# Optimization experiments

Measured on AMD Instinct MI355X. Metric: run time of the kernel, lower is better.

Reference implementation:

```python
import jax, jax.numpy as jnp
import numpy as np

B, S, E, H = 2, 2048, 1024, 16
D = E // H  # head size = 64


def setup_inputs() -> dict:
    key = jax.random.key(0)
    ks = jax.random.split(key, 13)
    scale = 1.0 / np.sqrt(E)
    inp = {
        "q": jax.random.normal(ks[0], (B, S, E), jnp.float32),
        "k": jax.random.normal(ks[1], (B, S, E), jnp.float32),
        "v": jax.random.normal(ks[2], (B, S, E), jnp.float32),
        "mask": jax.random.randint(ks[3], (B, 1, S, S), 0, 2, jnp.int32),
        "Wq": jax.random.normal(ks[4], (E, E), jnp.float32) * scale,
        "bq": jnp.zeros((E,), jnp.float32),
        "Wk": jax.random.normal(ks[5], (E, E), jnp.float32) * scale,
        "bk": jnp.zeros((E,), jnp.float32),
        "Wv": jax.random.normal(ks[6], (E, E), jnp.float32) * scale,
        "bv": jnp.zeros((E,), jnp.float32),
        "Wo": jax.random.normal(ks[7], (E, E), jnp.float32) * scale,
        "bo": jnp.zeros((E,), jnp.float32),
    }
    return inp


def reference(q, k, v, mask, Wq, bq, Wk, bk, Wv, bv, Wo, bo):
    # Linear projections (torch Linear: x @ W.T + b)
    qh = (q @ Wq.T + bq).reshape(B, S, H, D).transpose(0, 2, 1, 3)  # [B,H,S,D]
    kh = (k @ Wk.T + bk).reshape(B, S, H, D).transpose(0, 2, 1, 3)
    vh = (v @ Wv.T + bv).reshape(B, S, H, D).transpose(0, 2, 1, 3)

    scores = jnp.einsum("bhqd,bhkd->bhqk", qh, kh) / jnp.sqrt(jnp.float32(D))
    scores = jnp.where(mask == 0, jnp.float32(-1e10), scores)
    attn = jax.nn.softmax(scores, axis=-1)  # [B,H,S,S]
    ctx = jnp.einsum("bhqk,bhkd->bhqd", attn, vh)  # dropout p=0.0 -> identity

    out = ctx.transpose(0, 2, 1, 3).reshape(B, S, E)
    return out @ Wo.T + bo
```

## Files before the change

kernel.cpp:

```cpp
#include <hip/hip_runtime.h>

typedef unsigned short ushort_t;
typedef __attribute__((ext_vector_type(8))) short short8;
typedef __attribute__((ext_vector_type(4))) float f32x4;
typedef __attribute__((ext_vector_type(4))) unsigned short ushort4_t;
typedef __attribute__((ext_vector_type(4))) unsigned int uint4_t;

#define BB 2
#define SS 2048
#define EE 1024
#define HH 16
#define DD 64
#define MM (BB*SS)

#define QB_OFF  0u
#define KB_OFF  4194304u
#define VB_OFF  8388608u
#define WQ_OFF  12582912u
#define WK_OFF  13631488u
#define WV_OFF  14680064u
#define WO_OFF  15728640u
#define QH_OFF  16777216u
#define KH_OFF  20971520u
#define VT_OFF  25165824u
#define CTX_OFF QB_OFF
#define MB_OFF  29360128u

__device__ __forceinline__ ushort_t f2bf(float x) {
    unsigned u = __builtin_bit_cast(unsigned, x);
    u += 0x7FFFu + ((u >> 16) & 1u);
    return (ushort_t)(u >> 16);
}

__device__ __forceinline__ unsigned cvt_pk_bf16(float a, float b) {
    unsigned r;
    asm("v_cvt_pk_bf16_f32 %0, %1, %2" : "=v"(r) : "v"(a), "v"(b));
    return r;
}

__device__ __forceinline__ void load_lds16(const void* g, void* l) {
    __builtin_amdgcn_global_load_lds((const __attribute__((address_space(1))) void*)g,
                                     (__attribute__((address_space(3))) void*)l, 16, 0, 0);
}

__global__ __launch_bounds__(256) void prep_kernel(
    const float* __restrict__ q, const float* __restrict__ k, const float* __restrict__ v,
    const int* __restrict__ mask,
    const float* __restrict__ Wq, const float* __restrict__ Wk,
    const float* __restrict__ Wv, const float* __restrict__ Wo,
    ushort_t* __restrict__ wsb, unsigned* __restrict__ maskbits)
{
    int g = blockIdx.x;
    if (g < 16384) {
        int idx = g * 256 + threadIdx.x;
        const float* src; ushort_t* dst; int rel;
        if      (idx < 1048576) { src = q;  dst = wsb + QB_OFF; rel = idx; }
        else if (idx < 2097152) { src = k;  dst = wsb + KB_OFF; rel = idx - 1048576; }
        else if (idx < 3145728) { src = v;  dst = wsb + VB_OFF; rel = idx - 2097152; }
        else if (idx < 3407872) { src = Wq; dst = wsb + WQ_OFF; rel = idx - 3145728; }
        else if (idx < 3670016) { src = Wk; dst = wsb + WK_OFF; rel = idx - 3407872; }
        else if (idx < 3932160) { src = Wv; dst = wsb + WV_OFF; rel = idx - 3670016; }
        else                    { src = Wo; dst = wsb + WO_OFF; rel = idx - 3932160; }
        f32x4 val = ((const f32x4*)src)[rel];
        ushort4_t o;
        o.x = f2bf(val.x); o.y = f2bf(val.y); o.z = f2bf(val.z); o.w = f2bf(val.w);
        ((ushort4_t*)dst)[rel] = o;
    } else {
        const int lane = threadIdx.x & 63;
        int wid = (g - 16384) * 4 + (threadIdx.x >> 6);
        int row = wid >> 2, seg = wid & 3;
        int b = row >> 11, qr = row & 2047;
        const int* mp = mask + ((size_t)b * SS + qr) * SS + seg * 512;
        unsigned* outw = maskbits + ((size_t)b * SS + qr) * 64 + seg * 16;
        #pragma unroll
        for (int i = 0; i < 8; ++i) {
            unsigned long long bal = __ballot(mp[i * 64 + lane] != 0);
            if (lane == 0) {
                outw[i * 2]     = (unsigned)bal;
                outw[i * 2 + 1] = (unsigned)(bal >> 32);
            }
        }
    }
}

__device__ __forceinline__ void gemm_mainloop(
    const ushort_t* __restrict__ A, const ushort_t* __restrict__ Bm,
    int m0, int n0, f32x4 acc[4][4], ushort_t* As, ushort_t* Bs)
{
    const int tid  = threadIdx.x;
    const int wave = tid >> 6, lane = tid & 63;
    const int r16  = lane >> 2;
    const int c8   = (lane & 3) * 8;
    const int lane15 = lane & 15, quad = lane >> 4;
    const int wm = wave >> 1, wn = wave & 1;

    #pragma unroll 1
    for (int kt = 0; kt < 16; ++kt) {
        const int k0 = kt * 64;
        __syncthreads();
        #pragma unroll
        for (int s = 0; s < 2; ++s) {
            const ushort_t* ga = A  + (size_t)(m0 + wave * 32 + r16) * 1024 + k0 + s * 32 + c8;
            load_lds16(ga,             As + s * 4096 + wave * 1024);
            load_lds16(ga + 16 * 1024, As + s * 4096 + wave * 1024 + 512);
            const ushort_t* gb = Bm + (size_t)(n0 + wave * 32 + r16) * 1024 + k0 + s * 32 + c8;
            load_lds16(gb,             Bs + s * 4096 + wave * 1024);
            load_lds16(gb + 16 * 1024, Bs + s * 4096 + wave * 1024 + 512);
        }
        __syncthreads();

        #pragma unroll
        for (int s = 0; s < 2; ++s) {
            short8 a[4], bf[4];
            #pragma unroll
            for (int i = 0; i < 4; ++i)
                a[i] = *(const short8*)&As[s * 4096 + (wm * 64 + i * 16 + lane15) * 32 + quad * 8];
            #pragma unroll
            for (int j = 0; j < 4; ++j)
                bf[j] = *(const short8*)&Bs[s * 4096 + (wn * 64 + j * 16 + lane15) * 32 + quad * 8];
            #pragma unroll
            for (int i = 0; i < 4; ++i)
                #pragma unroll
                for (int j = 0; j < 4; ++j)
                    acc[i][j] = __builtin_amdgcn_mfma_f32_16x16x32_bf16(a[i], bf[j], acc[i][j], 0, 0, 0);
        }
    }
}

__global__ __launch_bounds__(256) void gemm_qkv(
    ushort_t* __restrict__ wsb,
    const float* __restrict__ bq, const float* __restrict__ bk, const float* __restrict__ bv)
{
    __shared__ ushort_t As[2 * 4096], Bs[2 * 4096];
    const int z = blockIdx.z;
    const ushort_t* A;
    const ushort_t* Bm;
    if      (z == 0) { A = wsb + QB_OFF; Bm = wsb + WQ_OFF; }
    else if (z == 1) { A = wsb + KB_OFF; Bm = wsb + WK_OFF; }
    else             { A = wsb + WV_OFF; Bm = wsb + VB_OFF; }
    const float* bias  = (z == 0) ? bq : (z == 1) ? bk : bv;
    ushort_t* dst      = wsb + (z == 0 ? QH_OFF : z == 1 ? KH_OFF : VT_OFF);
    const int m0 = (z < 2) ? blockIdx.y * 128 : blockIdx.x * 128;
    const int n0 = (z < 2) ? blockIdx.x * 128 : blockIdx.y * 128;

    f32x4 acc[4][4];
    #pragma unroll
    for (int i = 0; i < 4; ++i)
        #pragma unroll
        for (int j = 0; j < 4; ++j) acc[i][j] = (f32x4){0.f, 0.f, 0.f, 0.f};

    gemm_mainloop(A, Bm, m0, n0, acc, As, Bs);

    const int tid = threadIdx.x, wave = tid >> 6, lane = tid & 63;
    const int lane15 = lane & 15, quad = lane >> 4;
    const int wm = wave >> 1, wn = wave & 1;
    const float scale = (z == 0) ? 0.180336880111f : 1.0f;

    if (z < 2) {
        #pragma unroll
        for (int i = 0; i < 4; ++i) {
            #pragma unroll
            for (int j = 0; j < 4; ++j) {
                int col = n0 + wn * 64 + j * 16 + lane15;
                float bv_ = bias[col];
                int hh = col >> 6, d = col & 63;
                #pragma unroll
                for (int r = 0; r < 4; ++r) {
                    int row = m0 + wm * 64 + i * 16 + quad * 4 + r;
                    int bb = row >> 11, s = row & 2047;
                    float val = (acc[i][j][r] + bv_) * scale;
                    dst[(((size_t)bb * HH + hh) * SS + s) * DD + d] = f2bf(val);
                }
            }
        }
    } else {
        #pragma unroll
        for (int i = 0; i < 4; ++i) {
            #pragma unroll
            for (int r = 0; r < 4; ++r) {
                int row = m0 + wm * 64 + i * 16 + quad * 4 + r;
                float bv_ = bias[row];
                int hh = row >> 6, d = row & 63;
                #pragma unroll
                for (int j = 0; j < 4; ++j) {
                    int col = n0 + wn * 64 + j * 16 + lane15;
                    int bb = col >> 11, s = col & 2047;
                    int kk = s & 127;
                    int sp = (kk & 0x60) | ((kk & 12) << 1) | ((kk & 16) >> 2) | (kk & 3);
                    dst[(((size_t)bb * HH + hh) * DD + d) * SS + (s & ~127) + sp]
                        = f2bf(acc[i][j][r] + bv_);
                }
            }
        }
    }
}

__global__ __launch_bounds__(256, 2) void attn_kernel(
    const ushort_t* __restrict__ wsb, const unsigned* __restrict__ maskbits,
    ushort_t* __restrict__ ctx)
{
    __shared__ ushort_t Ks[128 * 64];
    __shared__ ushort_t Vts[64 * 128];

    const int tid  = threadIdx.x;
    const int wave = tid >> 6, lane = tid & 63;
    const int lane15 = lane & 15, quad = lane >> 4;
    const int sw7 = lane15 & 7;
    const int bh = blockIdx.y;
    const int b  = bh >> 4, h = bh & 15;
    const int q0 = blockIdx.x * 128;

    const ushort_t* Qh  = wsb + QH_OFF;
    const ushort_t* Kh  = wsb + KH_OFF;
    const ushort_t* VhT = wsb + VT_OFF;

    short8 qfrag[2][2];
    #pragma unroll
    for (int i = 0; i < 2; ++i)
        #pragma unroll
        for (int ks = 0; ks < 2; ++ks)
            qfrag[i][ks] = *(const short8*)(Qh +
                ((size_t)bh * SS + q0 + wave * 32 + i * 16 + lane15) * DD + ks * 32 + quad * 8);

    short8 ones_frag;
    {
        short onev = (lane15 == 0) ? (short)0x3F80 : (short)0;
        #pragma unroll
        for (int e = 0; e < 8; ++e) ones_frag[e] = onev;
    }

    const f32x4 zero4 = (f32x4){0.f, 0.f, 0.f, 0.f};
    f32x4 s_acc[2][8];
    f32x4 o_acc[2][4];
    f32x4 osum[2];
    #pragma unroll
    for (int i = 0; i < 2; ++i) {
        #pragma unroll
        for (int jd = 0; jd < 4; ++jd) o_acc[i][jd] = zero4;
        osum[i] = zero4;
    }

    #pragma unroll 1
    for (int kt = 0; kt < 16; ++kt) {
        const int k0 = kt * 128;
        __syncthreads();

        const ushort_t* Kbase = Kh + ((size_t)bh * SS + k0) * DD;
        #pragma unroll
        for (int cc = 0; cc < 4; ++cc) {
            int n = (wave * 4 + cc) * 64 + lane;
            int row = n >> 3;
            int c = (n & 7) ^ (row & 7);
            load_lds16(Kbase + row * 64 + c * 8, Ks + (wave * 4 + cc) * 512);
        }
        const ushort_t* Vbase = VhT + ((size_t)bh * DD) * SS + k0;
        #pragma unroll
        for (int cc = 0; cc < 4; ++cc) {
            int n = (wave * 4 + cc) * 64 + lane;
            int d = n >> 4;
            int c = (n & 15) ^ (d & 7);
            load_lds16(Vbase + (size_t)d * SS + c * 8, Vts + (wave * 4 + cc) * 512);
        }

        unsigned mw2[2][4];
        {
            const int kw0 = k0 >> 5;
            #pragma unroll
            for (int i = 0; i < 2; ++i) {
                const size_t qrow = (size_t)b * SS + q0 + wave * 32 + i * 16 + lane15;
                #pragma unroll
                for (int w = 0; w < 4; ++w)
                    mw2[i][w] = maskbits[qrow * 64 + kw0 + w];
            }
        }
        __syncthreads();

        #pragma unroll
        for (int j = 0; j < 8; ++j) {
            short8 kf = *(const short8*)&Ks[(j * 16 + lane15) * 64 + ((quad ^ sw7) << 3)];
            s_acc[0][j] = __builtin_amdgcn_mfma_f32_16x16x32_bf16(kf, qfrag[0][0], zero4, 0, 0, 0);
            s_acc[1][j] = __builtin_amdgcn_mfma_f32_16x16x32_bf16(kf, qfrag[1][0], zero4, 0, 0, 0);
        }
        #pragma unroll
        for (int j = 0; j < 8; ++j) {
            short8 kf = *(const short8*)&Ks[(j * 16 + lane15) * 64 + (((4 + quad) ^ sw7) << 3)];
            s_acc[0][j] = __builtin_amdgcn_mfma_f32_16x16x32_bf16(kf, qfrag[0][1], s_acc[0][j], 0, 0, 0);
            s_acc[1][j] = __builtin_amdgcn_mfma_f32_16x16x32_bf16(kf, qfrag[1][1], s_acc[1][j], 0, 0, 0);
        }

        #pragma unroll
        for (int ks = 0; ks < 4; ++ks) {
            short8 ap[2];
            #pragma unroll
            for (int i = 0; i < 2; ++i) {
                float p[2][4];
                #pragma unroll
                for (int hf = 0; hf < 2; ++hf) {
                    #pragma unroll
                    for (int r = 0; r < 4; ++r) {
                        float e = __builtin_amdgcn_exp2f(s_acc[i][ks * 2 + hf][r]);
                        p[hf][r] = ((mw2[i][ks] >> (hf * 16 + quad * 4 + r)) & 1u) ? e : 0.f;
                    }
                }
                uint4_t api;
                api.x = cvt_pk_bf16(p[0][0], p[0][1]);
                api.y = cvt_pk_bf16(p[0][2], p[0][3]);
                api.z = cvt_pk_bf16(p[1][0], p[1][1]);
                api.w = cvt_pk_bf16(p[1][2], p[1][3]);
                ap[i] = __builtin_bit_cast(short8, api);
            }
            #pragma unroll
            for (int jd = 0; jd < 4; ++jd) {
                short8 bv_ = *(const short8*)&Vts[(jd * 16 + lane15) * 128 +
                                                  (((ks * 4 + quad) ^ sw7) << 3)];
                o_acc[0][jd] = __builtin_amdgcn_mfma_f32_16x16x32_bf16(ap[0], bv_, o_acc[0][jd], 0, 0, 0);
                o_acc[1][jd] = __builtin_amdgcn_mfma_f32_16x16x32_bf16(ap[1], bv_, o_acc[1][jd], 0, 0, 0);
            }
            osum[0] = __builtin_amdgcn_mfma_f32_16x16x32_bf16(ap[0], ones_frag, osum[0], 0, 0, 0);
            osum[1] = __builtin_amdgcn_mfma_f32_16x16x32_bf16(ap[1], ones_frag, osum[1], 0, 0, 0);
        }
    }

    #pragma unroll
    for (int i = 0; i < 2; ++i) {
        #pragma unroll
        for (int r = 0; r < 4; ++r) {
            float l = __shfl(osum[i][r], lane & 48);
            float inv = 1.0f / l;
            int row = q0 + wave * 32 + i * 16 + quad * 4 + r;
            #pragma unroll
            for (int jd = 0; jd < 4; ++jd) {
                int col = h * DD + jd * 16 + lane15;
                ctx[((size_t)b * SS + row) * EE + col] = f2bf(o_acc[i][jd][r] * inv);
            }
        }
    }
}

__global__ __launch_bounds__(256) void gemm_out(
    const ushort_t* __restrict__ wsb, const float* __restrict__ bo, float* __restrict__ out)
{
    __shared__ ushort_t As[4 * 2048];
    __shared__ ushort_t Bs[4 * 4096];
    const ushort_t* A  = wsb + CTX_OFF;
    const ushort_t* Bm = wsb + WO_OFF;
    const int m0 = blockIdx.y * 64, n0 = blockIdx.x * 128;

    const int tid = threadIdx.x, wave = tid >> 6, lane = tid & 63;
    const int lane15 = lane & 15, quad = lane >> 4;

    f32x4 acc[8];
    #pragma unroll
    for (int j = 0; j < 8; ++j) acc[j] = (f32x4){0.f, 0.f, 0.f, 0.f};

    #pragma unroll 1
    for (int kt = 0; kt < 8; ++kt) {
        const int k0 = kt * 128;
        __syncthreads();
        #pragma unroll
        for (int s = 0; s < 4; ++s) {
            {
                int n = wave * 64 + lane;
                load_lds16(A + (size_t)(m0 + (n >> 2)) * 1024 + k0 + s * 32 + (n & 3) * 8,
                           As + s * 2048 + wave * 512);
            }
            #pragma unroll
            for (int m = 0; m < 2; ++m) {
                int n = m * 256 + wave * 64 + lane;
                load_lds16(Bm + (size_t)(n0 + (n >> 2)) * 1024 + k0 + s * 32 + (n & 3) * 8,
                           Bs + s * 4096 + (m * 256 + wave * 64) * 8);
            }
        }
        __syncthreads();

        #pragma unroll
        for (int s = 0; s < 4; ++s) {
            short8 a = *(const short8*)&As[s * 2048 + (wave * 16 + lane15) * 32 + quad * 8];
            #pragma unroll
            for (int j = 0; j < 8; ++j) {
                short8 bf = *(const short8*)&Bs[s * 4096 + (j * 16 + lane15) * 32 + quad * 8];
                acc[j] = __builtin_amdgcn_mfma_f32_16x16x32_bf16(a, bf, acc[j], 0, 0, 0);
            }
        }
    }

    #pragma unroll
    for (int j = 0; j < 8; ++j) {
        int col = n0 + j * 16 + lane15;
        float bv_ = bo[col];
        #pragma unroll
        for (int r = 0; r < 4; ++r) {
            int row = m0 + wave * 16 + quad * 4 + r;
            out[(size_t)row * EE + col] = acc[j][r] + bv_;
        }
    }
}

extern "C" void kernel_launch(void* const* d_in, const int* in_sizes, int n_in,
                              void* d_out, int out_size, void* d_ws, size_t ws_size,
                              hipStream_t stream) {
    const float* q    = (const float*)d_in[0];
    const float* k    = (const float*)d_in[1];
    const float* v    = (const float*)d_in[2];
    const int*   mask = (const int*)  d_in[3];
    const float* Wq   = (const float*)d_in[4];
    const float* bq   = (const float*)d_in[5];
    const float* Wk   = (const float*)d_in[6];
    const float* bk   = (const float*)d_in[7];
    const float* Wv   = (const float*)d_in[8];
    const float* bv   = (const float*)d_in[9];
    const float* Wo   = (const float*)d_in[10];
    const float* bo   = (const float*)d_in[11];

    ushort_t* wsb = (ushort_t*)d_ws;
    unsigned* maskbits = (unsigned*)(wsb + MB_OFF);

    prep_kernel<<<20480, 256, 0, stream>>>(q, k, v, mask, Wq, Wk, Wv, Wo, wsb, maskbits);
    gemm_qkv<<<dim3(8, 32, 3), 256, 0, stream>>>(wsb, bq, bk, bv);
    attn_kernel<<<dim3(16, 32), 256, 0, stream>>>(wsb, maskbits, wsb + CTX_OFF);
    gemm_out<<<dim3(8, 64), 256, 0, stream>>>(wsb, bo, (float*)d_out);
}
```

Before: 261.0 us.

## Double-buffer K/V tiles in LDS to prefetch next tile during compute

The attention kernel now holds two LDS buffers each for K and V. The next key tile's async global-to-LDS loads are issued before the current tile's QK^T, softmax and PV math, and the second barrier per iteration is dropped. The aim is to hide global load latency behind MFMA work. In exchange, LDS use per block doubles to 64 KB, which may limit occupancy, and correctness relies on the top-of-loop barrier draining the outstanding async loads.

```diff
diff --git a/kernel.cpp b/kernel.cpp
--- a/kernel.cpp
+++ b/kernel.cpp
@@ -199,8 +199,8 @@
     const ushort_t* __restrict__ wsb, const unsigned* __restrict__ maskbits,
     ushort_t* __restrict__ ctx)
 {
-    __shared__ ushort_t Ks[128 * 64];
-    __shared__ ushort_t Vts[64 * 128];
+    __shared__ ushort_t Ks[2][128 * 64];
+    __shared__ ushort_t Vts[2][64 * 128];
 
     const int tid  = threadIdx.x;
     const int wave = tid >> 6, lane = tid & 63;
@@ -210,9 +210,9 @@
     const int b  = bh >> 4, h = bh & 15;
     const int q0 = blockIdx.x * 128;
 
-    const ushort_t* Qh  = wsb + QH_OFF;
-    const ushort_t* Kh  = wsb + KH_OFF;
-    const ushort_t* VhT = wsb + VT_OFF;
+    const ushort_t* Qh     = wsb + QH_OFF;
+    const ushort_t* Kbase0 = wsb + KH_OFF + (size_t)bh * SS * DD;
+    const ushort_t* Vbase0 = wsb + VT_OFF + (size_t)bh * DD * SS;
 
     short8 qfrag[2][2];
     #pragma unroll
@@ -240,31 +240,29 @@
         osum[i] = zero4;
     }
 
+    #pragma unroll
+    for (int cc = 0; cc < 4; ++cc) {
+        int n = (wave * 4 + cc) * 64 + lane;
+        int row = n >> 3;
+        int c = (n & 7) ^ (row & 7);
+        load_lds16(Kbase0 + row * 64 + c * 8, &Ks[0][(wave * 4 + cc) * 512]);
+    }
+    #pragma unroll
+    for (int cc = 0; cc < 4; ++cc) {
+        int n = (wave * 4 + cc) * 64 + lane;
+        int d = n >> 4;
+        int c = (n & 15) ^ (d & 7);
+        load_lds16(Vbase0 + (size_t)d * SS + c * 8, &Vts[0][(wave * 4 + cc) * 512]);
+    }
+
     #pragma unroll 1
     for (int kt = 0; kt < 16; ++kt) {
-        const int k0 = kt * 128;
+        const int cur = kt & 1;
         __syncthreads();
-
-        const ushort_t* Kbase = Kh + ((size_t)bh * SS + k0) * DD;
-        #pragma unroll
-        for (int cc = 0; cc < 4; ++cc) {
-            int n = (wave * 4 + cc) * 64 + lane;
-            int row = n >> 3;
-            int c = (n & 7) ^ (row & 7);
-            load_lds16(Kbase + row * 64 + c * 8, Ks + (wave * 4 + cc) * 512);
-        }
-        const ushort_t* Vbase = VhT + ((size_t)bh * DD) * SS + k0;
-        #pragma unroll
-        for (int cc = 0; cc < 4; ++cc) {
-            int n = (wave * 4 + cc) * 64 + lane;
-            int d = n >> 4;
-            int c = (n & 15) ^ (d & 7);
-            load_lds16(Vbase + (size_t)d * SS + c * 8, Vts + (wave * 4 + cc) * 512);
-        }
 
         unsigned mw2[2][4];
         {
-            const int kw0 = k0 >> 5;
+            const int kw0 = (kt * 128) >> 5;
             #pragma unroll
             for (int i = 0; i < 2; ++i) {
                 const size_t qrow = (size_t)b * SS + q0 + wave * 32 + i * 16 + lane15;
@@ -273,17 +271,37 @@
                     mw2[i][w] = maskbits[qrow * 64 + kw0 + w];
             }
         }
-        __syncthreads();
+        if (kt < 15) {
+            const ushort_t* Kb = Kbase0 + (size_t)(kt + 1) * 128 * DD;
+            const ushort_t* Vb = Vbase0 + (kt + 1) * 128;
+            #pragma unroll
+            for (int cc = 0; cc < 4; ++cc) {
+                int n = (wave * 4 + cc) * 64 + lane;
+                int row = n >> 3;
+                int c = (n & 7) ^ (row & 7);
+                load_lds16(Kb + row * 64 + c * 8, &Ks[cur ^ 1][(wave * 4 + cc) * 512]);
+            }
+            #pragma unroll
+            for (int cc = 0; cc < 4; ++cc) {
+                int n = (wave * 4 + cc) * 64 + lane;
+                int d = n >> 4;
+                int c = (n & 15) ^ (d & 7);
+                load_lds16(Vb + (size_t)d * SS + c * 8, &Vts[cur ^ 1][(wave * 4 + cc) * 512]);
+            }
+        }
+
+        const ushort_t* ksr = &Ks[cur][0];
+        const ushort_t* vsr = &Vts[cur][0];
 
         #pragma unroll
         for (int j = 0; j < 8; ++j) {
-            short8 kf = *(const short8*)&Ks[(j * 16 + lane15) * 64 + ((quad ^ sw7) << 3)];
+            short8 kf = *(const short8*)&ksr[(j * 16 + lane15) * 64 + ((quad ^ sw7) << 3)];
             s_acc[0][j] = __builtin_amdgcn_mfma_f32_16x16x32_bf16(kf, qfrag[0][0], zero4, 0, 0, 0);
             s_acc[1][j] = __builtin_amdgcn_mfma_f32_16x16x32_bf16(kf, qfrag[1][0], zero4, 0, 0, 0);
         }
         #pragma unroll
         for (int j = 0; j < 8; ++j) {
-            short8 kf = *(const short8*)&Ks[(j * 16 + lane15) * 64 + (((4 + quad) ^ sw7) << 3)];
+            short8 kf = *(const short8*)&ksr[(j * 16 + lane15) * 64 + (((4 + quad) ^ sw7) << 3)];
             s_acc[0][j] = __builtin_amdgcn_mfma_f32_16x16x32_bf16(kf, qfrag[0][1], s_acc[0][j], 0, 0, 0);
             s_acc[1][j] = __builtin_amdgcn_mfma_f32_16x16x32_bf16(kf, qfrag[1][1], s_acc[1][j], 0, 0, 0);
         }
@@ -311,7 +329,7 @@
             }
             #pragma unroll
             for (int jd = 0; jd < 4; ++jd) {
-                short8 bv_ = *(const short8*)&Vts[(jd * 16 + lane15) * 128 +
+                short8 bv_ = *(const short8*)&vsr[(jd * 16 + lane15) * 128 +
                                                   (((ks * 4 + quad) ^ sw7) << 3)];
                 o_acc[0][jd] = __builtin_amdgcn_mfma_f32_16x16x32_bf16(ap[0], bv_, o_acc[0][jd], 0, 0, 0);
                 o_acc[1][jd] = __builtin_amdgcn_mfma_f32_16x16x32_bf16(ap[1], bv_, o_acc[1][jd], 0, 0, 0);
```

New measurement: 264.8 us. No clear change (+1.5%).
